# Optimization experiments

Measured on AMD Instinct MI355X. Metric: run time of the kernel, lower is better.

The kernel has to match this reference:

```python
import jax, jax.numpy as jnp
import numpy as np

M = 30000          # number of internal octree nodes
N = 2              # branching factor per axis (N3Tree)
S = N ** 3         # children per node
D = 32             # data_dim
DEPTH_LIMIT = 10
MLP_RATIO = 2
L = 7 * M + 1      # number of leaf cells: 8*M - (M-1)


def _build_tree(seed=0):
    """Random recursive octree: parent_pack[i] = packed (parent_node,x,y,z) of node i."""
    rng = np.random.default_rng(seed)
    parent_pack = np.zeros(M, np.int32)
    node_depth = np.zeros(M, np.int32)
    occupied = np.zeros((M, S), bool)
    free = [(0, c) for c in range(S)]  # refinable cells (keeps child depth <= DEPTH_LIMIT-1)
    for i in range(1, M):
        j = int(rng.integers(len(free)))
        p, c = free[j]
        free[j] = free[-1]
        free.pop()
        occupied[p, c] = True
        parent_pack[i] = p * S + c
        node_depth[i] = node_depth[p] + 1
        if node_depth[i] <= DEPTH_LIMIT - 2:
            free.extend((i, c2) for c2 in range(S))
    leaf_idx = np.flatnonzero(~occupied.reshape(-1)).astype(np.int32)
    assert leaf_idx.shape[0] == L
    return parent_pack, node_depth, leaf_idx


def setup_inputs() -> dict:
    parent_pack, node_depth, leaf_idx = _build_tree()
    # torch.sort(parent_depth, dim=0, descending=True) sorts each column independently
    idx_sorted = np.sort(parent_pack)[::-1].copy()
    depth_sorted = np.sort(node_depth)[::-1].copy()
    key = jax.random.key(0)
    ks = jax.random.split(key, 8)
    H = D * MLP_RATIO
    return {
        "data": jax.random.normal(ks[0], (M, N, N, N, D), jnp.float32),
        "conv_w": jax.random.normal(ks[1], (DEPTH_LIMIT, D, D, S), jnp.float32) * 0.05,
        "conv_b": jnp.zeros((DEPTH_LIMIT, D), jnp.float32),
        "depth_weight": jnp.arange(1, DEPTH_LIMIT + 1, dtype=jnp.float32) / (DEPTH_LIMIT + 1),
        "hf_w1": jax.random.normal(ks[2], (D, H), jnp.float32) * 0.02,
        "hf_b1": jnp.zeros((H,), jnp.float32),
        "hf_w2": jax.random.normal(ks[3], (H, 3), jnp.float32) * 0.02,
        "hf_b2": jnp.zeros((3,), jnp.float32),
        "hs_w1": jax.random.normal(ks[4], (D, H), jnp.float32) * 0.02,
        "hs_b1": jnp.zeros((H,), jnp.float32),
        "hs_w2": jax.random.normal(ks[5], (H, 1), jnp.float32) * 0.02,
        "hs_b2": jnp.zeros((1,), jnp.float32),
        "idx_sorted": jnp.asarray(idx_sorted),
        "depth_sorted": jnp.asarray(depth_sorted),
        "node_depth": jnp.asarray(node_depth),
        "leaf_idx": jnp.asarray(leaf_idx),
    }


def _mlp(x, w1, b1, w2, b2):
    # timm Mlp (Linear-GELU-Drop-Linear-Drop), dropout is identity in eval
    return jax.nn.gelu(x @ w1 + b1, approximate=False) @ w2 + b2


def reference(data, conv_w, conv_b, depth_weight,
              hf_w1, hf_b1, hf_w2, hf_b2,
              hs_w1, hs_b1, hs_w2, hs_b2,
              idx_sorted, depth_sorted, node_depth, leaf_idx):
    Dd = data.shape[-1]

    def step(carry, inp):
        dat, feats = carry
        idx, dsort = inp
        p = idx // S
        cell = idx % S
        x, y, z = cell // (N * N), (cell // N) % N, cell % N
        blk = dat[p].reshape(S, Dd)            # [(N1 N2 N3), D]
        cd = node_depth[p]                     # conv chosen by node's own depth entry
        # TreeConv over the 8-cell block: y[o] = sum_{i,k} W[o,i,k] * x[i,k] + b[o]
        feat = jnp.einsum('oik,ki->o', conv_w[cd], blk) + conv_b[cd]
        dat = dat.at[p, x, y, z].set(feat)     # recursive scatter write into tree.data
        feats = feats + depth_weight[dsort] * feat
        return (dat, feats), None

    (data, feats), _ = jax.lax.scan(
        step, (data, jnp.zeros((Dd,), data.dtype)), (idx_sorted, depth_sorted))

    leaves = data.reshape(-1, Dd)[leaf_idx] + feats   # tree[:] + features, [L, D]
    f = _mlp(leaves, hf_w1, hf_b1, hf_w2, hf_b2)      # [L, 3]
    sigma = _mlp(leaves, hs_w1, hs_b1, hs_w2, hs_b2)  # [L, 1]
    return jnp.concatenate([f, sigma], axis=1)        # [L, 4]
```

## Files before the change

### kernel.cpp

```cpp
#include <hip/hip_runtime.h>
#include <hip/hip_bf16.h>
#include <math.h>


typedef __attribute__((ext_vector_type(8))) short short8;
typedef __attribute__((ext_vector_type(4))) float f32x4;

#define WT_N 81920
#define RCAP 30720
#define RSTRIDE 32
#define FSLOTS 256

__device__ __forceinline__ unsigned short f2bf(float x) {
    __hip_bfloat16 h = __float2bfloat16(x);
    return *reinterpret_cast<unsigned short*>(&h);
}
__device__ __forceinline__ float bf2f(unsigned short h) {
    union { float f; unsigned u; } v; v.u = ((unsigned)h) << 16;
    return v.f;
}

__device__ __forceinline__ float4 shfl4(float4 v, int src) {
    float4 r;
    r.x = __shfl(v.x, src, 64);
    r.y = __shfl(v.y, src, 64);
    r.z = __shfl(v.z, src, 64);
    r.w = __shfl(v.w, src, 64);
    return r;
}

__device__ __forceinline__ void red_ig(float4& T) {
    #pragma unroll
    for (int m = 8; m <= 32; m <<= 1) {
        T.x += __shfl_xor(T.x, m, 64);
        T.y += __shfl_xor(T.y, m, 64);
        T.z += __shfl_xor(T.z, m, 64);
        T.w += __shfl_xor(T.w, m, 64);
    }
}

__device__ __forceinline__ float gelu_fast(float x)
{
    float e = __expf(-1.702f * x);
    return x * __builtin_amdgcn_rcpf(1.0f + e);
}

__global__ __launch_bounds__(256) void zero_kernel(int* __restrict__ dst)
{
    int i = blockIdx.x * 256 + threadIdx.x;
    if (i < 10 * RSTRIDE) dst[i] = 0;
}

__global__ __launch_bounds__(256) void prep_kernel(
    const float* __restrict__ conv_w, float* __restrict__ Wt,
    const float* __restrict__ hf_w1, const float* __restrict__ hs_w1,
    short* __restrict__ bph, short* __restrict__ bpl,
    const int* __restrict__ idx_sorted, const int* __restrict__ node_depth,
    int* __restrict__ gcnt, int2* __restrict__ runlist,
    float* __restrict__ feats_part, int M)
{
    __shared__ float tl[32 * 257];
    __shared__ int hcnt[16], hbase[16];

    if (blockIdx.x < 10) {
        int d = blockIdx.x;
        int base = d * 8192;
        for (int t = threadIdx.x; t < 8192; t += 256)
            tl[(t >> 8) * 257 + (t & 255)] = conv_w[base + t];
        __syncthreads();
        for (int t = threadIdx.x; t < 8192; t += 256) {
            int o = t & 31, i = (t >> 5) & 31, k = t >> 10;
            Wt[base + t] = tl[o * 257 + i * 8 + k];
        }
        return;
    }

    if (threadIdx.x < 16) hcnt[threadIdx.x] = 0;
    __syncthreads();

    int j = (blockIdx.x - 10) * 256 + threadIdx.x;
    bool start = false;
    int d = 0, myp = 0, mypos = 0;

    if (j < M) {
        int p = idx_sorted[j] >> 3;
        start = (j == 0) || ((idx_sorted[j - 1] >> 3) != p);
        if (start) {
            d = node_depth[p];
            myp = p;
            mypos = atomicAdd(&hcnt[d], 1);
        }
    } else if (j < M + 512) {
        int jj = j - M;
        int lane = jj & 63;
        int q = jj >> 6;
        int m = q >> 2, tq = q & 3;
        int kg = lane >> 4, n0 = lane & 15, k0 = kg * 8;
        const float* __restrict__ w1 = m ? hs_w1 : hf_w1;
        #pragma unroll
        for (int i = 0; i < 8; ++i) {
            float w = w1[(k0 + i) * 64 + tq * 16 + n0];
            unsigned short hh = f2bf(w);
            bph[(q * 64 + lane) * 8 + i] = (short)hh;
            bpl[(q * 64 + lane) * 8 + i] = (short)f2bf(w - bf2f(hh));
        }
    } else if (j < M + 512 + FSLOTS * 32) {
        feats_part[j - (M + 512)] = 0.0f;
    }

    __syncthreads();
    if (threadIdx.x < 16) {
        int c = hcnt[threadIdx.x];
        if (c > 0) hbase[threadIdx.x] = atomicAdd(&gcnt[threadIdx.x * RSTRIDE], c);
    }
    __syncthreads();
    if (start) runlist[d * RCAP + hbase[d] + mypos] = make_int2(j, myp);
}

__device__ __forceinline__ void run_steps(
    float4& T, float4& blk, float4& pfs, int ec, float edw, int base16,
    int n, int p, bool valid, const float* __restrict__ W, float4 bias,
    int og, int og8, int ig, float* __restrict__ patch)
{
    if (!valid) return;
    int c = __shfl(ec, base16, 64);
    float4 wc0 = *(const float4*)(W + (c * 32 + ig * 4 + 0) * 32 + og);
    float4 wc1 = *(const float4*)(W + (c * 32 + ig * 4 + 1) * 32 + og);
    float4 wc2 = *(const float4*)(W + (c * 32 + ig * 4 + 2) * 32 + og);
    float4 wc3 = *(const float4*)(W + (c * 32 + ig * 4 + 3) * 32 + og);

    for (int s = 0;; ++s) {
        float dw = __shfl(edw, base16 + s, 64);
        float4 feat = {T.x + bias.x, T.y + bias.y, T.z + bias.z, T.w + bias.w};
        pfs.x = fmaf(dw, feat.x, pfs.x); pfs.y = fmaf(dw, feat.y, pfs.y);
        pfs.z = fmaf(dw, feat.z, pfs.z); pfs.w = fmaf(dw, feat.w, pfs.w);

        if (s + 1 == n) {
            if (p == 0 && c == 0 && ig == 0)
                *(float4*)(patch + og) = feat;
            return;
        }

        int cn = __shfl(ec, base16 + s + 1, 64);
        float4 nw0 = *(const float4*)(W + (cn * 32 + ig * 4 + 0) * 32 + og);
        float4 nw1 = *(const float4*)(W + (cn * 32 + ig * 4 + 1) * 32 + og);
        float4 nw2 = *(const float4*)(W + (cn * 32 + ig * 4 + 2) * 32 + og);
        float4 nw3 = *(const float4*)(W + (cn * 32 + ig * 4 + 3) * 32 + og);

        float4 ov = shfl4(blk, c * 8 + og8);
        float4 du = {feat.x - ov.x, feat.y - ov.y, feat.z - ov.z, feat.w - ov.w};
        if (ig == c) blk = feat;
        float4 u = shfl4(du, og8 * 8 + ig);

        float4 a4;
        a4.x = u.x * wc0.x; a4.y = u.x * wc0.y;
        a4.z = u.x * wc0.z; a4.w = u.x * wc0.w;
        a4.x = fmaf(u.y, wc1.x, a4.x); a4.y = fmaf(u.y, wc1.y, a4.y);
        a4.z = fmaf(u.y, wc1.z, a4.z); a4.w = fmaf(u.y, wc1.w, a4.w);
        a4.x = fmaf(u.z, wc2.x, a4.x); a4.y = fmaf(u.z, wc2.y, a4.y);
        a4.z = fmaf(u.z, wc2.z, a4.z); a4.w = fmaf(u.z, wc2.w, a4.w);
        a4.x = fmaf(u.w, wc3.x, a4.x); a4.y = fmaf(u.w, wc3.y, a4.y);
        a4.z = fmaf(u.w, wc3.z, a4.z); a4.w = fmaf(u.w, wc3.w, a4.w);
        red_ig(a4);
        T.x += a4.x; T.y += a4.y; T.z += a4.z; T.w += a4.w;

        c = cn;
        wc0 = nw0; wc1 = nw1; wc2 = nw2; wc3 = nw3;
    }
}

#define FMA16(T, X) \
    T.x = fmaf(X.x, w0.x, T.x); T.y = fmaf(X.x, w0.y, T.y); \
    T.z = fmaf(X.x, w0.z, T.z); T.w = fmaf(X.x, w0.w, T.w); \
    T.x = fmaf(X.y, w1.x, T.x); T.y = fmaf(X.y, w1.y, T.y); \
    T.z = fmaf(X.y, w1.z, T.z); T.w = fmaf(X.y, w1.w, T.w); \
    T.x = fmaf(X.z, w2.x, T.x); T.y = fmaf(X.z, w2.y, T.y); \
    T.z = fmaf(X.z, w2.z, T.z); T.w = fmaf(X.z, w2.w, T.w); \
    T.x = fmaf(X.w, w3.x, T.x); T.y = fmaf(X.w, w3.y, T.y); \
    T.z = fmaf(X.w, w3.z, T.z); T.w = fmaf(X.w, w3.w, T.w);

__global__ __launch_bounds__(256, 4) void conv_scan(
    const float* __restrict__ data, const float* __restrict__ Wt,
    const float* __restrict__ conv_b, const float* __restrict__ depth_weight,
    const int* __restrict__ idx_sorted, const int* __restrict__ depth_sorted,
    const int* __restrict__ gcnt, const int2* __restrict__ runlist,
    float* __restrict__ feats_part, float* __restrict__ patch, int M)
{
    __shared__ float fred[4][32];

    int w = (blockIdx.x * 256 + threadIdx.x) >> 6;
    int l = threadIdx.x & 63;
    int wv = threadIdx.x >> 6;
    int og8 = l & 7, og = og8 * 4, ig = l >> 3;
    int q = l >> 4;

    int acc = 0, d = -1, chunk = 0, cnt = 0;
    #pragma unroll
    for (int dd = 0; dd < 10; ++dd) {
        int c = gcnt[dd * RSTRIDE];
        int nw = (c + 3) >> 2;
        if (d < 0 && w < acc + nw) { d = dd; chunk = w - acc; cnt = c; }
        acc += nw;
    }

    float4 pfs = {0, 0, 0, 0};
    if (d >= 0) {
        int r0 = chunk * 4;
        int rq = r0 + q; if (rq >= cnt) rq = cnt - 1;
        int2 e = runlist[d * RCAP + rq];
        int t0l = e.x, pl = e.y;

        int wl = l & 15;
        int tw = t0l + wl;
        int twc = tw < M ? tw : M - 1;
        int iw  = idx_sorted[twc];
        int dsw = depth_sorted[twc];
        unsigned long long mask = __ballot((tw < M) && ((iw >> 3) == pl));
        int   ec  = iw & 7;
        float edw = depth_weight[dsw & 15];

        const float* __restrict__ W = Wt + d * 8192;
        const float4 bias = *(const float4*)(conv_b + d * 32 + og);

        int p0 = __shfl(pl, 0, 64),  p1 = __shfl(pl, 16, 64),
            p2 = __shfl(pl, 32, 64), p3 = __shfl(pl, 48, 64);
        int n0 = __builtin_ctz(~(unsigned)( mask        & 0xFFFFull));
        int n1 = __builtin_ctz(~(unsigned)((mask >> 16) & 0xFFFFull));
        int n2 = __builtin_ctz(~(unsigned)((mask >> 32) & 0xFFFFull));
        int n3 = __builtin_ctz(~(unsigned)((mask >> 48) & 0xFFFFull));
        bool v0 = (r0 + 0 < cnt), v1 = (r0 + 1 < cnt),
             v2 = (r0 + 2 < cnt), v3 = (r0 + 3 < cnt);

        float4 B0 = *(const float4*)(data + (size_t)p0 * 256 + ig * 32 + og);
        float4 B1 = *(const float4*)(data + (size_t)p1 * 256 + ig * 32 + og);
        float4 B2 = *(const float4*)(data + (size_t)p2 * 256 + ig * 32 + og);
        float4 B3 = *(const float4*)(data + (size_t)p3 * 256 + ig * 32 + og);

        float4 T0 = {0,0,0,0}, T1 = {0,0,0,0}, T2 = {0,0,0,0}, T3 = {0,0,0,0};
        #pragma unroll
        for (int k = 0; k < 8; ++k) {
            const float4 w0 = *(const float4*)(W + (k * 32 + ig * 4 + 0) * 32 + og);
            const float4 w1 = *(const float4*)(W + (k * 32 + ig * 4 + 1) * 32 + og);
            const float4 w2 = *(const float4*)(W + (k * 32 + ig * 4 + 2) * 32 + og);
            const float4 w3 = *(const float4*)(W + (k * 32 + ig * 4 + 3) * 32 + og);
            float4 x0 = *(const float4*)(data + (size_t)p0 * 256 + k * 32 + ig * 4);
            float4 x1 = *(const float4*)(data + (size_t)p1 * 256 + k * 32 + ig * 4);
            float4 x2 = *(const float4*)(data + (size_t)p2 * 256 + k * 32 + ig * 4);
            float4 x3 = *(const float4*)(data + (size_t)p3 * 256 + k * 32 + ig * 4);
            FMA16(T0, x0); FMA16(T1, x1); FMA16(T2, x2); FMA16(T3, x3);
        }
        red_ig(T0); red_ig(T1); red_ig(T2); red_ig(T3);

        run_steps(T0, B0, pfs, ec, edw,  0, n0, p0, v0, W, bias, og, og8, ig, patch);
        run_steps(T1, B1, pfs, ec, edw, 16, n1, p1, v1, W, bias, og, og8, ig, patch);
        run_steps(T2, B2, pfs, ec, edw, 32, n2, p2, v2, W, bias, og, og8, ig, patch);
        run_steps(T3, B3, pfs, ec, edw, 48, n3, p3, v3, W, bias, og, og8, ig, patch);
    }

    if (ig == 0) {
        fred[wv][og + 0] = pfs.x;
        fred[wv][og + 1] = pfs.y;
        fred[wv][og + 2] = pfs.z;
        fred[wv][og + 3] = pfs.w;
    }
    __syncthreads();
    if (threadIdx.x < 32) {
        float s = fred[0][threadIdx.x] + fred[1][threadIdx.x]
                + fred[2][threadIdx.x] + fred[3][threadIdx.x];
        atomicAdd(&feats_part[(blockIdx.x & (FSLOTS - 1)) * 32 + threadIdx.x], s);
    }
}

__global__ __launch_bounds__(256, 4) void mlp_kernel(
    const float* __restrict__ data, const float* __restrict__ feats_part,
    const float* __restrict__ patch, const int* __restrict__ leaf_idx,
    const short* __restrict__ bph, const short* __restrict__ bpl,
    const float* __restrict__ hf_w1, const float* __restrict__ hs_w1,
    const float* __restrict__ hf_b1, const float* __restrict__ hf_w2,
    const float* __restrict__ hf_b2, const float* __restrict__ hs_b1,
    const float* __restrict__ hs_w2, const float* __restrict__ hs_b2,
    float* __restrict__ out, int L)
{
    __shared__ float red[256];
    __shared__ float sh_fts[32];
    __shared__ float sh_fvec[128];
    __shared__ __align__(16) short sh_b[4096];

    {
        int ch = threadIdx.x & 31, g = threadIdx.x >> 5;
        float s = 0.f;
        #pragma unroll
        for (int j = 0; j < FSLOTS / 8; ++j)
            s += feats_part[(g + j * 8) * 32 + ch];
        red[threadIdx.x] = s;
        __syncthreads();
        if (threadIdx.x < 128) red[threadIdx.x] += red[threadIdx.x + 128];
        __syncthreads();
        if (threadIdx.x < 64) red[threadIdx.x] += red[threadIdx.x + 64];
        __syncthreads();
        if (threadIdx.x < 32)
            sh_fts[threadIdx.x] = red[threadIdx.x] + red[threadIdx.x + 32];
        __syncthreads();
    }

    {
        const int4* src = (const int4*)bph;
        int4* dst = (int4*)sh_b;
        for (int t = threadIdx.x; t < 512; t += 256) dst[t] = src[t];

        if (threadIdx.x < 128) {
            int m = threadIdx.x >> 6, h = threadIdx.x & 63;
            const float* __restrict__ w1 = m ? hs_w1 : hf_w1;
            float s = 0.f;
            #pragma unroll
            for (int k = 0; k < 32; ++k) s = fmaf(sh_fts[k], w1[k * 64 + h], s);
            sh_fvec[threadIdx.x] = s;
        }
        __syncthreads();
    }

    int l = threadIdx.x & 63;
    int ck = blockIdx.x * 4 + (threadIdx.x >> 6);
    int nchunks = (L + 63) >> 6;
    if (ck >= nchunks) return;
    int base = ck * 64;
    int n0 = l & 15, kg = l >> 4, k0 = kg * 8;

    float w2r[16], b1r[8];
    #pragma unroll
    for (int t = 0; t < 4; ++t) {
        int h = t * 16 + n0;
        w2r[t * 4 + 0] = hf_w2[h * 3 + 0];
        w2r[t * 4 + 1] = hf_w2[h * 3 + 1];
        w2r[t * 4 + 2] = hf_w2[h * 3 + 2];
        w2r[t * 4 + 3] = hs_w2[h];
        b1r[t]     = hf_b1[h] + sh_fvec[h];
        b1r[4 + t] = hs_b1[h] + sh_fvec[64 + h];
    }
    float b20 = hf_b2[0], b21 = hf_b2[1], b22 = hf_b2[2], b23 = hs_b2[0];

    #pragma unroll
    for (int tm = 0; tm < 4; ++tm) {
        int r  = base + tm * 16 + n0;
        int rc = r < L ? r : L - 1;
        int row = leaf_idx[rc];
        const float* __restrict__ src = (row == 0) ? patch : (data + (size_t)row * 32);
        float4 vA = *(const float4*)(src + k0);
        float4 vB = *(const float4*)(src + k0 + 4);
        float xv[8] = {vA.x, vA.y, vA.z, vA.w, vB.x, vB.y, vB.z, vB.w};
        short8 ahi;
        #pragma unroll
        for (int i = 0; i < 8; ++i) ahi[i] = (short)f2bf(xv[i]);

        f32x4 acc[8];
        bool anyPatch = __any(row == 0);
        if (!anyPatch) {
            #pragma unroll
            for (int qq = 0; qq < 8; ++qq) {
                short8 bh = *(const short8*)(sh_b + (qq * 64 + l) * 8);
                float bv = b1r[qq];
                f32x4 a = (f32x4){bv, bv, bv, bv};
                acc[qq] = __builtin_amdgcn_mfma_f32_16x16x32_bf16(ahi, bh, a, 0, 0, 0);
            }
        } else {
            short8 alo;
            #pragma unroll
            for (int i = 0; i < 8; ++i) {
                unsigned short hh = (unsigned short)ahi[i];
                alo[i] = (short)f2bf(xv[i] - bf2f(hh));
            }
            #pragma unroll
            for (int qq = 0; qq < 8; ++qq) {
                short8 bh = *(const short8*)(sh_b + (qq * 64 + l) * 8);
                short8 bl = *(const short8*)(bpl + (qq * 64 + l) * 8);
                float bv = b1r[qq];
                f32x4 a = (f32x4){bv, bv, bv, bv};
                a = __builtin_amdgcn_mfma_f32_16x16x32_bf16(ahi, bh, a, 0, 0, 0);
                a = __builtin_amdgcn_mfma_f32_16x16x32_bf16(alo, bh, a, 0, 0, 0);
                a = __builtin_amdgcn_mfma_f32_16x16x32_bf16(ahi, bl, a, 0, 0, 0);
                acc[qq] = a;
            }
        }

        float o[4][4];
        #pragma unroll
        for (int g2 = 0; g2 < 4; ++g2) {
            #pragma unroll
            for (int c = 0; c < 4; ++c) o[g2][c] = 0.f;
        }
        #pragma unroll
        for (int t = 0; t < 4; ++t) {
            #pragma unroll
            for (int reg = 0; reg < 4; ++reg) {
                float gf = gelu_fast(acc[t][reg]);
                float gs = gelu_fast(acc[4 + t][reg]);
                o[reg][0] = fmaf(gf, w2r[t * 4 + 0], o[reg][0]);
                o[reg][1] = fmaf(gf, w2r[t * 4 + 1], o[reg][1]);
                o[reg][2] = fmaf(gf, w2r[t * 4 + 2], o[reg][2]);
                o[reg][3] = fmaf(gs, w2r[t * 4 + 3], o[reg][3]);
            }
        }
        #pragma unroll
        for (int mk = 1; mk < 16; mk <<= 1) {
            #pragma unroll
            for (int reg = 0; reg < 4; ++reg) {
                #pragma unroll
                for (int c = 0; c < 4; ++c)
                    o[reg][c] += __shfl_xor(o[reg][c], mk, 64);
            }
        }
        if (n0 < 4) {
            int rL = base + tm * 16 + kg * 4 + n0;
            if (rL < L) {
                float s0 = n0 == 0 ? o[0][0] : n0 == 1 ? o[1][0] : n0 == 2 ? o[2][0] : o[3][0];
                float s1 = n0 == 0 ? o[0][1] : n0 == 1 ? o[1][1] : n0 == 2 ? o[2][1] : o[3][1];
                float s2 = n0 == 0 ? o[0][2] : n0 == 1 ? o[1][2] : n0 == 2 ? o[2][2] : o[3][2];
                float s3 = n0 == 0 ? o[0][3] : n0 == 1 ? o[1][3] : n0 == 2 ? o[2][3] : o[3][3];
                float4 res = {s0 + b20, s1 + b21, s2 + b22, s3 + b23};
                *(float4*)(out + (size_t)rL * 4) = res;
            }
        }
    }
}

extern "C" void kernel_launch(void* const* d_in, const int* in_sizes, int n_in,
                              void* d_out, int out_size, void* d_ws, size_t ws_size,
                              hipStream_t stream)
{
    const float* data         = (const float*)d_in[0];
    const float* conv_w       = (const float*)d_in[1];
    const float* conv_b       = (const float*)d_in[2];
    const float* depth_weight = (const float*)d_in[3];
    const float* hf_w1        = (const float*)d_in[4];
    const float* hf_b1        = (const float*)d_in[5];
    const float* hf_w2        = (const float*)d_in[6];
    const float* hf_b2        = (const float*)d_in[7];
    const float* hs_w1        = (const float*)d_in[8];
    const float* hs_b1        = (const float*)d_in[9];
    const float* hs_w2        = (const float*)d_in[10];
    const float* hs_b2        = (const float*)d_in[11];
    const int*   idx_sorted   = (const int*)d_in[12];
    const int*   depth_sorted = (const int*)d_in[13];
    const int*   node_depth   = (const int*)d_in[14];
    const int*   leaf_idx     = (const int*)d_in[15];

    int M = in_sizes[12];
    int L = in_sizes[15];
    float* out = (float*)d_out;

    float* Wt         = (float*)d_ws;
    float* patch      = Wt + WT_N;
    short* bph        = (short*)(patch + 32);
    short* bpl        = bph + 4096;
    int*   gcnt       = (int*)(bpl + 4096);
    float* feats_part = (float*)(gcnt + 10 * RSTRIDE);
    int2*  runlist    = (int2*)(feats_part + FSLOTS * 32);

    zero_kernel<<<2, 256, 0, stream>>>(gcnt);

    int nb_prep = 10 + (M + 512 + FSLOTS * 32 + 255) / 256;
    prep_kernel<<<nb_prep, 256, 0, stream>>>(
        conv_w, Wt, hf_w1, hs_w1, bph, bpl,
        idx_sorted, node_depth, gcnt, runlist, feats_part, M);

    int max_waves = (M + 3) / 4 + 10;
    conv_scan<<<(max_waves + 3) / 4, 256, 0, stream>>>(
        data, Wt, conv_b, depth_weight, idx_sorted, depth_sorted,
        gcnt, runlist, feats_part, patch, M);

    int nchunks = (L + 63) / 64;
    mlp_kernel<<<(nchunks + 3) / 4, 256, 0, stream>>>(
        data, feats_part, patch, leaf_idx, bph, bpl,
        hf_w1, hs_w1,
        hf_b1, hf_w2, hf_b2, hs_b1, hs_w2, hs_b2, out, L);
}
```

Baseline: 57.81 us.

## Interleave four per-wave runs in lockstep and segregate single-step runs

The prep kernel now measures each run's length, stores it packed in the runlist, and partitions runs per depth into single-step runs (filled from the front) and multi-step runs (filled from the back). The conv kernel then processes the four runs of a wave in one interleaved loop up to the maximum length, predicating the incremental updates, instead of four sequential dependent loops. The aim is to raise instruction-level parallelism across independent runs and to group runs of similar length so less work is wasted. In exchange, every run in a wave pays for the longest run's iterations, and the shared counters now use two slots per depth.

After: 61.35 us. +6.1%, slower.

```diff
diff --git a/kernel.cpp b/kernel.cpp
--- a/kernel.cpp
+++ b/kernel.cpp
@@ -60,7 +60,7 @@
     float* __restrict__ feats_part, int M)
 {
     __shared__ float tl[32 * 257];
-    __shared__ int hcnt[16], hbase[16];
+    __shared__ int hcnt[32], hbase[32];
 
     if (blockIdx.x < 10) {
         int d = blockIdx.x;
@@ -75,20 +75,24 @@
         return;
     }
 
-    if (threadIdx.x < 16) hcnt[threadIdx.x] = 0;
+    if (threadIdx.x < 32) hcnt[threadIdx.x] = 0;
     __syncthreads();
 
     int j = (blockIdx.x - 10) * 256 + threadIdx.x;
     bool start = false;
-    int d = 0, myp = 0, mypos = 0;
+    int d = 0, myp = 0, myn = 1, seg = 0, mypos = 0;
 
     if (j < M) {
         int p = idx_sorted[j] >> 3;
         start = (j == 0) || ((idx_sorted[j - 1] >> 3) != p);
         if (start) {
+            int nn = 1;
+            while (nn < 9 && j + nn < M && (idx_sorted[j + nn] >> 3) == p) ++nn;
             d = node_depth[p];
             myp = p;
-            mypos = atomicAdd(&hcnt[d], 1);
+            myn = nn;
+            seg = (nn == 1) ? 0 : 1;
+            mypos = atomicAdd(&hcnt[d * 2 + seg], 1);
         }
     } else if (j < M + 512) {
         int jj = j - M;
@@ -109,63 +113,17 @@
     }
 
     __syncthreads();
-    if (threadIdx.x < 16) {
+    if (threadIdx.x < 20) {
         int c = hcnt[threadIdx.x];
-        if (c > 0) hbase[threadIdx.x] = atomicAdd(&gcnt[threadIdx.x * RSTRIDE], c);
+        if (c > 0)
+            hbase[threadIdx.x] =
+                atomicAdd(&gcnt[(threadIdx.x >> 1) * RSTRIDE + (threadIdx.x & 1)], c);
     }
     __syncthreads();
-    if (start) runlist[d * RCAP + hbase[d] + mypos] = make_int2(j, myp);
-}
-
-__device__ __forceinline__ void run_steps(
-    float4& T, float4& blk, float4& pfs, int ec, float edw, int base16,
-    int n, int p, bool valid, const float* __restrict__ W, float4 bias,
-    int og, int og8, int ig, float* __restrict__ patch)
-{
-    if (!valid) return;
-    int c = __shfl(ec, base16, 64);
-    float4 wc0 = *(const float4*)(W + (c * 32 + ig * 4 + 0) * 32 + og);
-    float4 wc1 = *(const float4*)(W + (c * 32 + ig * 4 + 1) * 32 + og);
-    float4 wc2 = *(const float4*)(W + (c * 32 + ig * 4 + 2) * 32 + og);
-    float4 wc3 = *(const float4*)(W + (c * 32 + ig * 4 + 3) * 32 + og);
-
-    for (int s = 0;; ++s) {
-        float dw = __shfl(edw, base16 + s, 64);
-        float4 feat = {T.x + bias.x, T.y + bias.y, T.z + bias.z, T.w + bias.w};
-        pfs.x = fmaf(dw, feat.x, pfs.x); pfs.y = fmaf(dw, feat.y, pfs.y);
-        pfs.z = fmaf(dw, feat.z, pfs.z); pfs.w = fmaf(dw, feat.w, pfs.w);
-
-        if (s + 1 == n) {
-            if (p == 0 && c == 0 && ig == 0)
-                *(float4*)(patch + og) = feat;
-            return;
-        }
-
-        int cn = __shfl(ec, base16 + s + 1, 64);
-        float4 nw0 = *(const float4*)(W + (cn * 32 + ig * 4 + 0) * 32 + og);
-        float4 nw1 = *(const float4*)(W + (cn * 32 + ig * 4 + 1) * 32 + og);
-        float4 nw2 = *(const float4*)(W + (cn * 32 + ig * 4 + 2) * 32 + og);
-        float4 nw3 = *(const float4*)(W + (cn * 32 + ig * 4 + 3) * 32 + og);
-
-        float4 ov = shfl4(blk, c * 8 + og8);
-        float4 du = {feat.x - ov.x, feat.y - ov.y, feat.z - ov.z, feat.w - ov.w};
-        if (ig == c) blk = feat;
-        float4 u = shfl4(du, og8 * 8 + ig);
-
-        float4 a4;
-        a4.x = u.x * wc0.x; a4.y = u.x * wc0.y;
-        a4.z = u.x * wc0.z; a4.w = u.x * wc0.w;
-        a4.x = fmaf(u.y, wc1.x, a4.x); a4.y = fmaf(u.y, wc1.y, a4.y);
-        a4.z = fmaf(u.y, wc1.z, a4.z); a4.w = fmaf(u.y, wc1.w, a4.w);
-        a4.x = fmaf(u.z, wc2.x, a4.x); a4.y = fmaf(u.z, wc2.y, a4.y);
-        a4.z = fmaf(u.z, wc2.z, a4.z); a4.w = fmaf(u.z, wc2.w, a4.w);
-        a4.x = fmaf(u.w, wc3.x, a4.x); a4.y = fmaf(u.w, wc3.y, a4.y);
-        a4.z = fmaf(u.w, wc3.z, a4.z); a4.w = fmaf(u.w, wc3.w, a4.w);
-        red_ig(a4);
-        T.x += a4.x; T.y += a4.y; T.z += a4.z; T.w += a4.w;
-
-        c = cn;
-        wc0 = nw0; wc1 = nw1; wc2 = nw2; wc3 = nw3;
+    if (start) {
+        int b = hbase[d * 2 + seg] + mypos;
+        int idx = (seg == 0) ? b : (RCAP - 1 - b);
+        runlist[d * RCAP + idx] = make_int2(j | (myn << 16), myp);
     }
 }
 
@@ -179,6 +137,25 @@
     T.x = fmaf(X.w, w3.x, T.x); T.y = fmaf(X.w, w3.y, T.y); \
     T.z = fmaf(X.w, w3.z, T.z); T.w = fmaf(X.w, w3.w, T.w);
 
+#define RUN_UPD(Tj, Bj, fj, cj, cnj, uj) \
+    { \
+        const float4 w0 = *(const float4*)(W + (cj * 32 + ig * 4 + 0) * 32 + og); \
+        const float4 w1 = *(const float4*)(W + (cj * 32 + ig * 4 + 1) * 32 + og); \
+        const float4 w2 = *(const float4*)(W + (cj * 32 + ig * 4 + 2) * 32 + og); \
+        const float4 w3 = *(const float4*)(W + (cj * 32 + ig * 4 + 3) * 32 + og); \
+        float4 ov = shfl4(Bj, cj * 8 + og8); \
+        float gg = uj ? 1.f : 0.f; \
+        float4 du = {(fj.x - ov.x) * gg, (fj.y - ov.y) * gg, \
+                     (fj.z - ov.z) * gg, (fj.w - ov.w) * gg}; \
+        if (uj && ig == cj) Bj = fj; \
+        float4 ub = shfl4(du, og8 * 8 + ig); \
+        float4 a4 = {0.f, 0.f, 0.f, 0.f}; \
+        FMA16(a4, ub); \
+        red_ig(a4); \
+        Tj.x += a4.x; Tj.y += a4.y; Tj.z += a4.z; Tj.w += a4.w; \
+        cj = uj ? cnj : cj; \
+    }
+
 __global__ __launch_bounds__(256, 4) void conv_scan(
     const float* __restrict__ data, const float* __restrict__ Wt,
     const float* __restrict__ conv_b, const float* __restrict__ depth_weight,
@@ -194,28 +171,33 @@
     int og8 = l & 7, og = og8 * 4, ig = l >> 3;
     int q = l >> 4;
 
-    int acc = 0, d = -1, chunk = 0, cnt = 0;
+    int acc = 0, d = -1, chunk = 0, cA = 0, cB = 0;
     #pragma unroll
     for (int dd = 0; dd < 10; ++dd) {
-        int c = gcnt[dd * RSTRIDE];
-        int nw = (c + 3) >> 2;
-        if (d < 0 && w < acc + nw) { d = dd; chunk = w - acc; cnt = c; }
+        int a = gcnt[dd * RSTRIDE];
+        int b = gcnt[dd * RSTRIDE + 1];
+        int nw = (a + b + 3) >> 2;
+        if (d < 0 && w < acc + nw) { d = dd; chunk = w - acc; cA = a; cB = b; }
         acc += nw;
     }
 
     float4 pfs = {0, 0, 0, 0};
     if (d >= 0) {
+        int slots = cA + cB;
         int r0 = chunk * 4;
-        int rq = r0 + q; if (rq >= cnt) rq = cnt - 1;
-        int2 e = runlist[d * RCAP + rq];
-        int t0l = e.x, pl = e.y;
+        int rr = r0 + q;
+        if (rr >= slots) rr = slots - 1;
+        int idx = (rr < cA) ? rr : (RCAP - 1 - (rr - cA));
+        int2 e = runlist[d * RCAP + idx];
+        int t0l = e.x & 0xFFFF;
+        int nlq = (e.x >> 16) & 15;
+        int pl  = e.y;
 
         int wl = l & 15;
         int tw = t0l + wl;
         int twc = tw < M ? tw : M - 1;
         int iw  = idx_sorted[twc];
         int dsw = depth_sorted[twc];
-        unsigned long long mask = __ballot((tw < M) && ((iw >> 3) == pl));
         int   ec  = iw & 7;
         float edw = depth_weight[dsw & 15];
 
@@ -224,12 +206,11 @@
 
         int p0 = __shfl(pl, 0, 64),  p1 = __shfl(pl, 16, 64),
             p2 = __shfl(pl, 32, 64), p3 = __shfl(pl, 48, 64);
-        int n0 = __builtin_ctz(~(unsigned)( mask        & 0xFFFFull));
-        int n1 = __builtin_ctz(~(unsigned)((mask >> 16) & 0xFFFFull));
-        int n2 = __builtin_ctz(~(unsigned)((mask >> 32) & 0xFFFFull));
-        int n3 = __builtin_ctz(~(unsigned)((mask >> 48) & 0xFFFFull));
-        bool v0 = (r0 + 0 < cnt), v1 = (r0 + 1 < cnt),
-             v2 = (r0 + 2 < cnt), v3 = (r0 + 3 < cnt);
+        int e0 = (r0 + 0 < slots) ? __shfl(nlq, 0, 64)  : 0;
+        int e1 = (r0 + 1 < slots) ? __shfl(nlq, 16, 64) : 0;
+        int e2 = (r0 + 2 < slots) ? __shfl(nlq, 32, 64) : 0;
+        int e3 = (r0 + 3 < slots) ? __shfl(nlq, 48, 64) : 0;
+        int nmax = max(max(e0, e1), max(e2, e3));
 
         float4 B0 = *(const float4*)(data + (size_t)p0 * 256 + ig * 32 + og);
         float4 B1 = *(const float4*)(data + (size_t)p1 * 256 + ig * 32 + og);
@@ -251,10 +232,51 @@
         }
         red_ig(T0); red_ig(T1); red_ig(T2); red_ig(T3);
 
-        run_steps(T0, B0, pfs, ec, edw,  0, n0, p0, v0, W, bias, og, og8, ig, patch);
-        run_steps(T1, B1, pfs, ec, edw, 16, n1, p1, v1, W, bias, og, og8, ig, patch);
-        run_steps(T2, B2, pfs, ec, edw, 32, n2, p2, v2, W, bias, og, og8, ig, patch);
-        run_steps(T3, B3, pfs, ec, edw, 48, n3, p3, v3, W, bias, og, og8, ig, patch);
+        int c0 = __shfl(ec, 0, 64),  c1 = __shfl(ec, 16, 64),
+            c2 = __shfl(ec, 32, 64), c3 = __shfl(ec, 48, 64);
+
+        for (int s = 0; s < nmax; ++s) {
+            float dw0 = __shfl(edw, 0 + s, 64);
+            float dw1 = __shfl(edw, 16 + s, 64);
+            float dw2 = __shfl(edw, 32 + s, 64);
+            float dw3 = __shfl(edw, 48 + s, 64);
+            float m0 = (s < e0) ? dw0 : 0.f;
+            float m1 = (s < e1) ? dw1 : 0.f;
+            float m2 = (s < e2) ? dw2 : 0.f;
+            float m3 = (s < e3) ? dw3 : 0.f;
+
+            float4 f0 = {T0.x + bias.x, T0.y + bias.y, T0.z + bias.z, T0.w + bias.w};
+            float4 f1 = {T1.x + bias.x, T1.y + bias.y, T1.z + bias.z, T1.w + bias.w};
+            float4 f2 = {T2.x + bias.x, T2.y + bias.y, T2.z + bias.z, T2.w + bias.w};
+            float4 f3 = {T3.x + bias.x, T3.y + bias.y, T3.z + bias.z, T3.w + bias.w};
+
+            pfs.x = fmaf(m0, f0.x, fmaf(m1, f1.x, fmaf(m2, f2.x, fmaf(m3, f3.x, pfs.x))));
+            pfs.y = fmaf(m0, f0.y, fmaf(m1, f1.y, fmaf(m2, f2.y, fmaf(m3, f3.y, pfs.y))));
+            pfs.z = fmaf(m0, f0.z, fmaf(m1, f1.z, fmaf(m2, f2.z, fmaf(m3, f3.z, pfs.z))));
+            pfs.w = fmaf(m0, f0.w, fmaf(m1, f1.w, fmaf(m2, f2.w, fmaf(m3, f3.w, pfs.w))));
+
+            if (ig == 0) {
+                if (s + 1 == e0 && p0 == 0 && c0 == 0) *(float4*)(patch + og) = f0;
+                if (s + 1 == e1 && p1 == 0 && c1 == 0) *(float4*)(patch + og) = f1;
+                if (s + 1 == e2 && p2 == 0 && c2 == 0) *(float4*)(patch + og) = f2;
+                if (s + 1 == e3 && p3 == 0 && c3 == 0) *(float4*)(patch + og) = f3;
+            }
+
+            bool u0 = (s + 1 < e0), u1 = (s + 1 < e1),
+                 u2 = (s + 1 < e2), u3 = (s + 1 < e3);
+            if (!(u0 | u1 | u2 | u3)) continue;
+
+            int sn = s + 1;
+            int cn0 = __shfl(ec, 0 + sn, 64);
+            int cn1 = __shfl(ec, 16 + sn, 64);
+            int cn2 = __shfl(ec, 32 + sn, 64);
+            int cn3 = __shfl(ec, 48 + sn, 64);
+
+            RUN_UPD(T0, B0, f0, c0, cn0, u0);
+            RUN_UPD(T1, B1, f1, c1, cn1, u1);
+            RUN_UPD(T2, B2, f2, c2, cn2, u2);
+            RUN_UPD(T3, B3, f3, c3, cn3, u3);
+        }
     }
 
     if (ig == 0) {
```
